# Optimization experiments

Hardware: AMD Instinct MI355X
Metric: run time of the kernel (lower is better)

Reference implementation:

```python
import jax, jax.numpy as jnp
import numpy as np

N, C, H, DIN = 200_000, 16, 64, 40  # nodes in level, max children, hidden_dim, input_dim+type_count
NEG = -1e9

def setup_inputs() -> dict:
    key = jax.random.key(0)
    ks = jax.random.split(key, 10)
    s = lambda k, shp, f=0.1: jax.random.normal(k, shp, jnp.float32) * f
    return {
        'node_features': jax.random.normal(ks[0], (N, 1, DIN), jnp.float32),
        'child_hiddens': jax.random.normal(ks[1], (N, C, H), jnp.float32),
        'A_c': jax.random.uniform(ks[2], (N, C, C), jnp.float32),  # edge present where > 0.5
        'child_count': jax.random.randint(ks[3], (N,), 1, C + 1, jnp.int32),
        'W': s(ks[4], (H, H)),
        'a_src': s(ks[5], (H,)),
        'a_dst': s(ks[6], (H,)),
        'Wx': s(ks[7], (DIN, 3 * H)),
        'Wh_g': s(ks[8], (H, 3 * H)),
        'b': jnp.zeros((3 * H,), jnp.float32),
    }

def reference(node_features, child_hiddens, A_c, child_count, W, a_src, a_dst, Wx, Wh_g, b):
    # --- GraphAttentionLayer over padded child adjacency ---
    Wh = jnp.einsum('nch,hk->nck', child_hiddens, W)            # [N,C,H]
    src = Wh @ a_src                                             # [N,C]
    dst = Wh @ a_dst                                             # [N,C]
    e = jax.nn.leaky_relu(src[:, :, None] + dst[:, None, :], 0.2)  # [N,C,C]
    valid = jnp.arange(C)[None, :] < child_count[:, None]        # [N,C] real (non-padded) children
    mask = (A_c > 0.5) & valid[:, None, :] & valid[:, :, None]
    attn = jax.nn.softmax(jnp.where(mask, e, NEG), axis=-1)
    h_msg = jax.nn.elu(jnp.einsum('nij,njh->nih', attn, Wh))     # [N,C,H]
    # --- MaxpoolReadoutLayer masked by child count ---
    pooled = jnp.max(jnp.where(valid[:, :, None], h_msg, NEG), axis=1, keepdims=True)  # [N,1,H]
    # --- GatedRecurrentUnit update ---
    gx = node_features @ Wx + b                                  # [N,1,3H]
    gh = pooled @ Wh_g                                           # [N,1,3H]
    xz, xr, xn = jnp.split(gx, 3, axis=-1)
    hz, hr, hn = jnp.split(gh, 3, axis=-1)
    z = jax.nn.sigmoid(xz + hz)
    r = jax.nn.sigmoid(xr + hr)
    n = jnp.tanh(xn + r * hn)
    hiddens = (1.0 - z) * n + z * pooled                         # [N,1,H]
    return hiddens
```

## Files before the change

### kernel.cpp

```cpp
#include <hip/hip_runtime.h>

typedef __attribute__((ext_vector_type(8))) short bf16x8;
typedef __attribute__((ext_vector_type(4))) float f32x4;

__device__ __forceinline__ unsigned short f2bf(float f) {
  unsigned u = __builtin_bit_cast(unsigned, f);
  u += 0x7fffu + ((u >> 16) & 1u);
  return (unsigned short)(u >> 16);
}
__device__ __forceinline__ float bf2f(unsigned short s) {
  unsigned u = ((unsigned)s) << 16;
  return __builtin_bit_cast(float, u);
}
__device__ __forceinline__ bf16x8 zero8() {
  bf16x8 r;
#pragma unroll
  for (int i = 0; i < 8; ++i) r[i] = 0;
  return r;
}

__global__ __launch_bounds__(256, 2) void rann_fused(
    const float* __restrict__ nf, const float* __restrict__ ch,
    const float* __restrict__ Ac, const int* __restrict__ ccnt,
    const float* __restrict__ W, const float* __restrict__ a_src,
    const float* __restrict__ a_dst, const float* __restrict__ Wx,
    const float* __restrict__ Whg, const float* __restrict__ bias,
    float* __restrict__ out, int N) {
  __shared__ __align__(16) unsigned short whgT[192][72];
  __shared__ __align__(16) unsigned short wxT[192][72];
  __shared__ __align__(16) float b_lds[192];
  __shared__ __align__(16) float srcdst[4][32];
  __shared__ __align__(16) unsigned short wh_t[4][64][16];
  __shared__ __align__(16) unsigned short pooledb[4][16][72];

  const int tid = threadIdx.x;
  for (int idx = tid; idx < 192 * 64; idx += 256) {
    const int col = idx % 192, k = idx / 192;
    whgT[col][k] = f2bf(Whg[k * 192 + col]);
    wxT[col][k] = (k < 40) ? f2bf(Wx[k * 192 + col]) : (unsigned short)0;
  }
  if (tid < 192) b_lds[tid] = bias[tid];
  __syncthreads();

  const int lane = tid & 63;
  const int w = tid >> 6;
  const int q = lane >> 4;
  const int m16 = lane & 15;

  bf16x8 wfrag[2][4];
#pragma unroll
  for (int t = 0; t < 2; ++t)
#pragma unroll
    for (int u = 0; u < 4; ++u) {
      bf16x8 f;
#pragma unroll
      for (int j = 0; j < 8; ++j)
        f[j] = (short)f2bf(W[(32 * t + 8 * q + j) * 64 + 16 * u + m16]);
      wfrag[t][u] = f;
    }
  float asv[4], adv[4];
#pragma unroll
  for (int u = 0; u < 4; ++u) {
    asv[u] = a_src[16 * u + m16];
    adv[u] = a_dst[16 * u + m16];
  }

  const int gwave = blockIdx.x * 4 + w;
  const int stride = gridDim.x * 4;
  const int nbatch = N >> 4;
  for (int bidx = gwave; bidx < nbatch; bidx += stride) {
    const int nb = bidx << 4;
    for (int s = 0; s < 16; ++s) {
      const int n = nb + s;
      const int cc = ccnt[n];
      bf16x8 afA[2];
#pragma unroll
      for (int t = 0; t < 2; ++t) {
        const float* p = ch + (size_t)n * 1024 + m16 * 64 + 32 * t + 8 * q;
        f32x4 v0 = *(const f32x4*)p;
        f32x4 v1 = *(const f32x4*)(p + 4);
        bf16x8 f;
#pragma unroll
        for (int j = 0; j < 4; ++j) {
          f[j] = (short)f2bf(v0[j]);
          f[j + 4] = (short)f2bf(v1[j]);
        }
        afA[t] = f;
      }
      f32x4 acc[4];
#pragma unroll
      for (int u = 0; u < 4; ++u) acc[u] = (f32x4){0.f, 0.f, 0.f, 0.f};
#pragma unroll
      for (int t = 0; t < 2; ++t)
#pragma unroll
        for (int u = 0; u < 4; ++u)
          acc[u] = __builtin_amdgcn_mfma_f32_16x16x32_bf16(afA[t], wfrag[t][u], acc[u], 0, 0, 0);

      float ps[4], pd[4];
#pragma unroll
      for (int r = 0; r < 4; ++r) {
        ps[r] = acc[0][r] * asv[0] + acc[1][r] * asv[1] + acc[2][r] * asv[2] + acc[3][r] * asv[3];
        pd[r] = acc[0][r] * adv[0] + acc[1][r] * adv[1] + acc[2][r] * adv[2] + acc[3][r] * adv[3];
      }
#pragma unroll
      for (int m = 1; m < 16; m <<= 1) {
#pragma unroll
        for (int r = 0; r < 4; ++r) {
          ps[r] += __shfl_xor(ps[r], m);
          pd[r] += __shfl_xor(pd[r], m);
        }
      }
      if (m16 == 0) {
        *(f32x4*)&srcdst[w][4 * q] = (f32x4){ps[0], ps[1], ps[2], ps[3]};
        *(f32x4*)&srcdst[w][16 + 4 * q] = (f32x4){pd[0], pd[1], pd[2], pd[3]};
      }
#pragma unroll
      for (int u = 0; u < 4; ++u) {
        uint2 v;
        v.x = (unsigned)f2bf(acc[u][0]) | ((unsigned)f2bf(acc[u][1]) << 16);
        v.y = (unsigned)f2bf(acc[u][2]) | ((unsigned)f2bf(acc[u][3]) << 16);
        *(uint2*)&wh_t[w][16 * u + m16][4 * q] = v;
      }
      __threadfence_block();

      const int qe = q & 1;
      const float srcv = srcdst[w][m16];
      f32x4 d0 = *(const f32x4*)&srcdst[w][16 + 8 * qe];
      f32x4 d1 = *(const f32x4*)&srcdst[w][16 + 8 * qe + 4];
      const float* ap = Ac + (size_t)n * 256 + m16 * 16 + 8 * qe;
      f32x4 a0 = *(const f32x4*)ap;
      f32x4 a1 = *(const f32x4*)(ap + 4);
      float p8[8];
      float rmax = -3.0e38f;
#pragma unroll
      for (int jj = 0; jj < 8; ++jj) {
        const float dstv = (jj < 4) ? d0[jj] : d1[jj - 4];
        const float av = (jj < 4) ? a0[jj] : a1[jj - 4];
        const float x = srcv + dstv;
        const float e = fmaxf(x, 0.2f * x);
        const bool msk = (av > 0.5f) && (m16 < cc) && ((8 * qe + jj) < cc);
        p8[jj] = msk ? e : -1.0e9f;
        rmax = fmaxf(rmax, p8[jj]);
      }
      rmax = fmaxf(rmax, __shfl_xor(rmax, 16));
      float psum = 0.f;
#pragma unroll
      for (int jj = 0; jj < 8; ++jj) {
        p8[jj] = __expf(p8[jj] - rmax);
        psum += p8[jj];
      }
      psum += __shfl_xor(psum, 16);
      const float inv = 1.0f / psum;
      bf16x8 afrag2 = zero8();
      if (q < 2) {
#pragma unroll
        for (int jj = 0; jj < 8; ++jj) afrag2[jj] = (short)f2bf(p8[jj] * inv);
      }
      f32x4 acc2[4];
#pragma unroll
      for (int u = 0; u < 4; ++u) {
        bf16x8 bf2 = zero8();
        if (q < 2) bf2 = *(const bf16x8*)&wh_t[w][16 * u + m16][8 * q];
        f32x4 z4 = (f32x4){0.f, 0.f, 0.f, 0.f};
        acc2[u] = __builtin_amdgcn_mfma_f32_16x16x32_bf16(afrag2, bf2, z4, 0, 0, 0);
      }
#pragma unroll
      for (int u = 0; u < 4; ++u) {
        float pm = -1.0e9f;
#pragma unroll
        for (int r = 0; r < 4; ++r) {
          const float v = acc2[u][r];
          const float ev = v > 0.f ? v : __expf(v) - 1.0f;
          pm = fmaxf(pm, (4 * q + r) < cc ? ev : -1.0e9f);
        }
        pm = fmaxf(pm, __shfl_xor(pm, 16));
        pm = fmaxf(pm, __shfl_xor(pm, 32));
        if (q == 0) pooledb[w][s][16 * u + m16] = f2bf(pm);
      }
    }
    __threadfence_block();

    bf16x8 afP[2];
#pragma unroll
    for (int t = 0; t < 2; ++t)
      afP[t] = *(const bf16x8*)&pooledb[w][m16][32 * t + 8 * q];
    bf16x8 afX[2];
    {
      const float* p = nf + (size_t)(nb + m16) * 40 + 8 * q;
      f32x4 v0 = *(const f32x4*)p;
      f32x4 v1 = *(const f32x4*)(p + 4);
      bf16x8 f;
#pragma unroll
      for (int j = 0; j < 4; ++j) {
        f[j] = (short)f2bf(v0[j]);
        f[j + 4] = (short)f2bf(v1[j]);
      }
      afX[0] = f;
      afX[1] = zero8();
      if (q == 0) {
        const float* p1 = nf + (size_t)(nb + m16) * 40 + 32;
        f32x4 w0 = *(const f32x4*)p1;
        f32x4 w1 = *(const f32x4*)(p1 + 4);
        bf16x8 g;
#pragma unroll
        for (int j = 0; j < 4; ++j) {
          g[j] = (short)f2bf(w0[j]);
          g[j + 4] = (short)f2bf(w1[j]);
        }
        afX[1] = g;
      }
    }
    f32x4 accS[8], accX4[4], accH4[4];
#pragma unroll
    for (int u = 0; u < 8; ++u) accS[u] = (f32x4){0.f, 0.f, 0.f, 0.f};
#pragma unroll
    for (int u = 0; u < 4; ++u) {
      accX4[u] = (f32x4){0.f, 0.f, 0.f, 0.f};
      accH4[u] = (f32x4){0.f, 0.f, 0.f, 0.f};
    }
#pragma unroll
    for (int u = 0; u < 8; ++u) {
      const int row = 16 * u + m16;
#pragma unroll
      for (int t = 0; t < 2; ++t) {
        accS[u] = __builtin_amdgcn_mfma_f32_16x16x32_bf16(
            afP[t], *(const bf16x8*)&whgT[row][32 * t + 8 * q], accS[u], 0, 0, 0);
        accS[u] = __builtin_amdgcn_mfma_f32_16x16x32_bf16(
            afX[t], *(const bf16x8*)&wxT[row][32 * t + 8 * q], accS[u], 0, 0, 0);
      }
    }
#pragma unroll
    for (int u = 0; u < 4; ++u) {
      const int row = 128 + 16 * u + m16;
#pragma unroll
      for (int t = 0; t < 2; ++t) {
        accH4[u] = __builtin_amdgcn_mfma_f32_16x16x32_bf16(
            afP[t], *(const bf16x8*)&whgT[row][32 * t + 8 * q], accH4[u], 0, 0, 0);
        accX4[u] = __builtin_amdgcn_mfma_f32_16x16x32_bf16(
            afX[t], *(const bf16x8*)&wxT[row][32 * t + 8 * q], accX4[u], 0, 0, 0);
      }
    }
#pragma unroll
    for (int u = 0; u < 4; ++u) {
      const int col = 16 * u + m16;
      const float bz = b_lds[col];
      const float br = b_lds[64 + col];
      const float bn = b_lds[128 + col];
#pragma unroll
      for (int r = 0; r < 4; ++r) {
        const int nl = 4 * q + r;
        const float z = 1.0f / (1.0f + __expf(-(accS[u][r] + bz)));
        const float rg = 1.0f / (1.0f + __expf(-(accS[u + 4][r] + br)));
        const float nn = tanhf(accX4[u][r] + bn + rg * accH4[u][r]);
        const float pv = bf2f(pooledb[w][nl][col]);
        out[(size_t)(nb + nl) * 64 + col] = (1.0f - z) * nn + z * pv;
      }
    }
  }
}

extern "C" void kernel_launch(void* const* d_in, const int* in_sizes, int n_in,
                              void* d_out, int out_size, void* d_ws, size_t ws_size,
                              hipStream_t stream) {
  const float* nf = (const float*)d_in[0];
  const float* ch = (const float*)d_in[1];
  const float* Ac = (const float*)d_in[2];
  const int* ccnt = (const int*)d_in[3];
  const float* W = (const float*)d_in[4];
  const float* a_src = (const float*)d_in[5];
  const float* a_dst = (const float*)d_in[6];
  const float* Wx = (const float*)d_in[7];
  const float* Whg = (const float*)d_in[8];
  const float* bias = (const float*)d_in[9];
  float* out = (float*)d_out;
  const int N = in_sizes[3];
  const int nbatch = N >> 4;
  int blocks = 625;
  if (blocks > (nbatch + 3) / 4) blocks = (nbatch + 3) / 4;
  if (blocks < 1) blocks = 1;
  hipLaunchKernelGGL(rann_fused, dim3(blocks), dim3(256), 0, stream,
                     nf, ch, Ac, ccnt, W, a_src, a_dst, Wx, Whg, bias, out, N);
}
```

Measured before the change: 1.500 ms.

## Split fused kernel into GAT-pool and GRU kernels with prefetch and folded attention vectors

```diff
diff --git a/kernel.cpp b/kernel.cpp
--- a/kernel.cpp
+++ b/kernel.cpp
@@ -8,9 +8,18 @@
   u += 0x7fffu + ((u >> 16) & 1u);
   return (unsigned short)(u >> 16);
 }
-__device__ __forceinline__ float bf2f(unsigned short s) {
-  unsigned u = ((unsigned)s) << 16;
-  return __builtin_bit_cast(float, u);
+__device__ __forceinline__ unsigned cvtpk(float lo, float hi) {
+  unsigned r;
+  asm("v_cvt_pk_bf16_f32 %0, %1, %2" : "=v"(r) : "v"(lo), "v"(hi));
+  return r;
+}
+__device__ __forceinline__ bf16x8 pk8(f32x4 a, f32x4 b) {
+  union { unsigned u[4]; bf16x8 v; } r;
+  r.u[0] = cvtpk(a[0], a[1]);
+  r.u[1] = cvtpk(a[2], a[3]);
+  r.u[2] = cvtpk(b[0], b[1]);
+  r.u[3] = cvtpk(b[2], b[3]);
+  return r.v;
 }
 __device__ __forceinline__ bf16x8 zero8() {
   bf16x8 r;
@@ -19,124 +28,106 @@
   return r;
 }
 
-__global__ __launch_bounds__(256, 2) void rann_fused(
-    const float* __restrict__ nf, const float* __restrict__ ch,
-    const float* __restrict__ Ac, const int* __restrict__ ccnt,
-    const float* __restrict__ W, const float* __restrict__ a_src,
-    const float* __restrict__ a_dst, const float* __restrict__ Wx,
-    const float* __restrict__ Whg, const float* __restrict__ bias,
-    float* __restrict__ out, int N) {
-  __shared__ __align__(16) unsigned short whgT[192][72];
-  __shared__ __align__(16) unsigned short wxT[192][72];
-  __shared__ __align__(16) float b_lds[192];
-  __shared__ __align__(16) float srcdst[4][32];
+__global__ __launch_bounds__(256, 3) void gat_pool(
+    const float* __restrict__ ch, const float* __restrict__ Ac,
+    const int* __restrict__ ccnt, const float* __restrict__ W,
+    const float* __restrict__ a_src, const float* __restrict__ a_dst,
+    float* __restrict__ pooled, int N) {
+  __shared__ __align__(16) unsigned short wT[64][72];
+  __shared__ __align__(16) float wa[128];
+  __shared__ __align__(16) float dstl[4][16];
   __shared__ __align__(16) unsigned short wh_t[4][64][16];
-  __shared__ __align__(16) unsigned short pooledb[4][16][72];
 
   const int tid = threadIdx.x;
-  for (int idx = tid; idx < 192 * 64; idx += 256) {
-    const int col = idx % 192, k = idx / 192;
-    whgT[col][k] = f2bf(Whg[k * 192 + col]);
-    wxT[col][k] = (k < 40) ? f2bf(Wx[k * 192 + col]) : (unsigned short)0;
-  }
-  if (tid < 192) b_lds[tid] = bias[tid];
+  for (int idx = tid; idx < 64 * 64; idx += 256) {
+    wT[idx & 63][idx >> 6] = f2bf(W[idx]);
+  }
+  if (tid < 128) {
+    const int k = tid & 63;
+    const float* av = (tid < 64) ? a_src : a_dst;
+    float s = 0.f;
+    for (int h = 0; h < 64; ++h) s += W[k * 64 + h] * av[h];
+    wa[tid] = s;
+  }
   __syncthreads();
 
   const int lane = tid & 63;
   const int w = tid >> 6;
   const int q = lane >> 4;
   const int m16 = lane & 15;
-
-  bf16x8 wfrag[2][4];
-#pragma unroll
-  for (int t = 0; t < 2; ++t)
-#pragma unroll
-    for (int u = 0; u < 4; ++u) {
-      bf16x8 f;
-#pragma unroll
-      for (int j = 0; j < 8; ++j)
-        f[j] = (short)f2bf(W[(32 * t + 8 * q + j) * 64 + 16 * u + m16]);
-      wfrag[t][u] = f;
-    }
-  float asv[4], adv[4];
-#pragma unroll
-  for (int u = 0; u < 4; ++u) {
-    asv[u] = a_src[16 * u + m16];
-    adv[u] = a_dst[16 * u + m16];
-  }
+  const int qe = q & 1;
+
+  const f32x4 ws0a = *(const f32x4*)&wa[8 * q];
+  const f32x4 ws0b = *(const f32x4*)&wa[8 * q + 4];
+  const f32x4 ws1a = *(const f32x4*)&wa[32 + 8 * q];
+  const f32x4 ws1b = *(const f32x4*)&wa[36 + 8 * q];
+  const f32x4 wd0a = *(const f32x4*)&wa[64 + 8 * q];
+  const f32x4 wd0b = *(const f32x4*)&wa[68 + 8 * q];
+  const f32x4 wd1a = *(const f32x4*)&wa[96 + 8 * q];
+  const f32x4 wd1b = *(const f32x4*)&wa[100 + 8 * q];
 
   const int gwave = blockIdx.x * 4 + w;
   const int stride = gridDim.x * 4;
   const int nbatch = N >> 4;
   for (int bidx = gwave; bidx < nbatch; bidx += stride) {
     const int nb = bidx << 4;
+    const float* pch = ch + (size_t)nb * 1024 + m16 * 64 + 8 * q;
+    const float* pac = Ac + (size_t)nb * 256 + m16 * 16 + 8 * qe;
+    const int ccv = ccnt[nb + m16];
+    f32x4 c0 = *(const f32x4*)pch;
+    f32x4 c1 = *(const f32x4*)(pch + 4);
+    f32x4 c2 = *(const f32x4*)(pch + 32);
+    f32x4 c3 = *(const f32x4*)(pch + 36);
+    f32x4 A0 = *(const f32x4*)pac;
+    f32x4 A1 = *(const f32x4*)(pac + 4);
+
     for (int s = 0; s < 16; ++s) {
       const int n = nb + s;
-      const int cc = ccnt[n];
-      bf16x8 afA[2];
-#pragma unroll
-      for (int t = 0; t < 2; ++t) {
-        const float* p = ch + (size_t)n * 1024 + m16 * 64 + 32 * t + 8 * q;
-        f32x4 v0 = *(const f32x4*)p;
-        f32x4 v1 = *(const f32x4*)(p + 4);
-        bf16x8 f;
-#pragma unroll
-        for (int j = 0; j < 4; ++j) {
-          f[j] = (short)f2bf(v0[j]);
-          f[j + 4] = (short)f2bf(v1[j]);
-        }
-        afA[t] = f;
-      }
+      const int cc = __builtin_amdgcn_readlane(ccv, s);
+      f32x4 nc0, nc1, nc2, nc3, nA0, nA1;
+      if (s < 15) {
+        const float* p2 = pch + (size_t)(s + 1) * 1024;
+        nc0 = *(const f32x4*)p2;
+        nc1 = *(const f32x4*)(p2 + 4);
+        nc2 = *(const f32x4*)(p2 + 32);
+        nc3 = *(const f32x4*)(p2 + 36);
+        const float* a2 = pac + (size_t)(s + 1) * 256;
+        nA0 = *(const f32x4*)a2;
+        nA1 = *(const f32x4*)(a2 + 4);
+      }
+      float ps = 0.f, pd = 0.f;
+#pragma unroll
+      for (int j = 0; j < 4; ++j) {
+        ps += c0[j] * ws0a[j] + c1[j] * ws0b[j] + c2[j] * ws1a[j] + c3[j] * ws1b[j];
+        pd += c0[j] * wd0a[j] + c1[j] * wd0b[j] + c2[j] * wd1a[j] + c3[j] * wd1b[j];
+      }
+      ps += __shfl_xor(ps, 16);
+      ps += __shfl_xor(ps, 32);
+      pd += __shfl_xor(pd, 16);
+      pd += __shfl_xor(pd, 32);
+      if (q == 0) dstl[w][m16] = pd;
+      const bf16x8 afA0 = pk8(c0, c1);
+      const bf16x8 afA1 = pk8(c2, c3);
       f32x4 acc[4];
 #pragma unroll
       for (int u = 0; u < 4; ++u) acc[u] = (f32x4){0.f, 0.f, 0.f, 0.f};
 #pragma unroll
-      for (int t = 0; t < 2; ++t)
-#pragma unroll
-        for (int u = 0; u < 4; ++u)
-          acc[u] = __builtin_amdgcn_mfma_f32_16x16x32_bf16(afA[t], wfrag[t][u], acc[u], 0, 0, 0);
-
-      float ps[4], pd[4];
-#pragma unroll
-      for (int r = 0; r < 4; ++r) {
-        ps[r] = acc[0][r] * asv[0] + acc[1][r] * asv[1] + acc[2][r] * asv[2] + acc[3][r] * asv[3];
-        pd[r] = acc[0][r] * adv[0] + acc[1][r] * adv[1] + acc[2][r] * adv[2] + acc[3][r] * adv[3];
-      }
-#pragma unroll
-      for (int m = 1; m < 16; m <<= 1) {
-#pragma unroll
-        for (int r = 0; r < 4; ++r) {
-          ps[r] += __shfl_xor(ps[r], m);
-          pd[r] += __shfl_xor(pd[r], m);
-        }
-      }
-      if (m16 == 0) {
-        *(f32x4*)&srcdst[w][4 * q] = (f32x4){ps[0], ps[1], ps[2], ps[3]};
-        *(f32x4*)&srcdst[w][16 + 4 * q] = (f32x4){pd[0], pd[1], pd[2], pd[3]};
-      }
-#pragma unroll
       for (int u = 0; u < 4; ++u) {
-        uint2 v;
-        v.x = (unsigned)f2bf(acc[u][0]) | ((unsigned)f2bf(acc[u][1]) << 16);
-        v.y = (unsigned)f2bf(acc[u][2]) | ((unsigned)f2bf(acc[u][3]) << 16);
-        *(uint2*)&wh_t[w][16 * u + m16][4 * q] = v;
+        acc[u] = __builtin_amdgcn_mfma_f32_16x16x32_bf16(
+            afA0, *(const bf16x8*)&wT[16 * u + m16][8 * q], acc[u], 0, 0, 0);
+        acc[u] = __builtin_amdgcn_mfma_f32_16x16x32_bf16(
+            afA1, *(const bf16x8*)&wT[16 * u + m16][32 + 8 * q], acc[u], 0, 0, 0);
       }
       __threadfence_block();
-
-      const int qe = q & 1;
-      const float srcv = srcdst[w][m16];
-      f32x4 d0 = *(const f32x4*)&srcdst[w][16 + 8 * qe];
-      f32x4 d1 = *(const f32x4*)&srcdst[w][16 + 8 * qe + 4];
-      const float* ap = Ac + (size_t)n * 256 + m16 * 16 + 8 * qe;
-      f32x4 a0 = *(const f32x4*)ap;
-      f32x4 a1 = *(const f32x4*)(ap + 4);
+      const f32x4 d0 = *(const f32x4*)&dstl[w][8 * qe];
+      const f32x4 d1 = *(const f32x4*)&dstl[w][8 * qe + 4];
       float p8[8];
       float rmax = -3.0e38f;
 #pragma unroll
       for (int jj = 0; jj < 8; ++jj) {
         const float dstv = (jj < 4) ? d0[jj] : d1[jj - 4];
-        const float av = (jj < 4) ? a0[jj] : a1[jj - 4];
-        const float x = srcv + dstv;
+        const float av = (jj < 4) ? A0[jj] : A1[jj - 4];
+        const float x = ps + dstv;
         const float e = fmaxf(x, 0.2f * x);
         const bool msk = (av > 0.5f) && (m16 < cc) && ((8 * qe + jj) < cc);
         p8[jj] = msk ? e : -1.0e9f;
@@ -153,63 +144,107 @@
       const float inv = 1.0f / psum;
       bf16x8 afrag2 = zero8();
       if (q < 2) {
-#pragma unroll
-        for (int jj = 0; jj < 8; ++jj) afrag2[jj] = (short)f2bf(p8[jj] * inv);
-      }
-      f32x4 acc2[4];
+        union { unsigned u[4]; bf16x8 v; } r;
+#pragma unroll
+        for (int jj = 0; jj < 4; ++jj)
+          r.u[jj] = cvtpk(p8[2 * jj] * inv, p8[2 * jj + 1] * inv);
+        afrag2 = r.v;
+      }
+#pragma unroll
+      for (int u = 0; u < 4; ++u) {
+        uint2 v;
+        v.x = cvtpk(acc[u][0], acc[u][1]);
+        v.y = cvtpk(acc[u][2], acc[u][3]);
+        *(uint2*)&wh_t[w][16 * u + m16][4 * q] = v;
+      }
+      __threadfence_block();
+      float pmv[4];
 #pragma unroll
       for (int u = 0; u < 4; ++u) {
         bf16x8 bf2 = zero8();
         if (q < 2) bf2 = *(const bf16x8*)&wh_t[w][16 * u + m16][8 * q];
-        f32x4 z4 = (f32x4){0.f, 0.f, 0.f, 0.f};
-        acc2[u] = __builtin_amdgcn_mfma_f32_16x16x32_bf16(afrag2, bf2, z4, 0, 0, 0);
-      }
-#pragma unroll
-      for (int u = 0; u < 4; ++u) {
+        const f32x4 z4 = (f32x4){0.f, 0.f, 0.f, 0.f};
+        const f32x4 h4 =
+            __builtin_amdgcn_mfma_f32_16x16x32_bf16(afrag2, bf2, z4, 0, 0, 0);
         float pm = -1.0e9f;
 #pragma unroll
         for (int r = 0; r < 4; ++r) {
-          const float v = acc2[u][r];
+          const float v = h4[r];
           const float ev = v > 0.f ? v : __expf(v) - 1.0f;
           pm = fmaxf(pm, (4 * q + r) < cc ? ev : -1.0e9f);
         }
         pm = fmaxf(pm, __shfl_xor(pm, 16));
         pm = fmaxf(pm, __shfl_xor(pm, 32));
-        if (q == 0) pooledb[w][s][16 * u + m16] = f2bf(pm);
-      }
-    }
-    __threadfence_block();
-
+        pmv[u] = pm;
+      }
+      const float sel = (q == 0) ? pmv[0] : (q == 1) ? pmv[1] : (q == 2) ? pmv[2] : pmv[3];
+      pooled[(size_t)n * 64 + lane] = sel;
+      if (s < 15) {
+        c0 = nc0; c1 = nc1; c2 = nc2; c3 = nc3;
+        A0 = nA0; A1 = nA1;
+      }
+    }
+  }
+}
+
+__global__ __launch_bounds__(256, 3) void gru_update(
+    const float* __restrict__ nf, const float* __restrict__ Wx,
+    const float* __restrict__ Whg, const float* __restrict__ bias,
+    float* hid, int N) {
+  __shared__ __align__(16) unsigned short whgT[192][72];
+  __shared__ __align__(16) unsigned short wxT[192][40];
+  __shared__ __align__(16) float b_lds[192];
+
+  const int tid = threadIdx.x;
+  for (int idx = tid; idx < 192 * 64; idx += 256) {
+    const int col = idx % 192, k = idx / 192;
+    whgT[col][k] = f2bf(Whg[k * 192 + col]);
+    if (k < 40) wxT[col][k] = f2bf(Wx[k * 192 + col]);
+  }
+  if (tid < 192) b_lds[tid] = bias[tid];
+  __syncthreads();
+
+  const int lane = tid & 63;
+  const int w = tid >> 6;
+  const int q = lane >> 4;
+  const int m16 = lane & 15;
+
+  const int gwave = blockIdx.x * 4 + w;
+  const int stride = gridDim.x * 4;
+  const int nbatch = N >> 4;
+  for (int bidx = gwave; bidx < nbatch; bidx += stride) {
+    const int nb = bidx << 4;
     bf16x8 afP[2];
-#pragma unroll
-    for (int t = 0; t < 2; ++t)
-      afP[t] = *(const bf16x8*)&pooledb[w][m16][32 * t + 8 * q];
+    {
+      const float* p = hid + (size_t)(nb + m16) * 64 + 8 * q;
+      const f32x4 v0 = *(const f32x4*)p;
+      const f32x4 v1 = *(const f32x4*)(p + 4);
+      const f32x4 v2 = *(const f32x4*)(p + 32);
+      const f32x4 v3 = *(const f32x4*)(p + 36);
+      afP[0] = pk8(v0, v1);
+      afP[1] = pk8(v2, v3);
+    }
     bf16x8 afX[2];
     {
       const float* p = nf + (size_t)(nb + m16) * 40 + 8 * q;
-      f32x4 v0 = *(const f32x4*)p;
-      f32x4 v1 = *(const f32x4*)(p + 4);
-      bf16x8 f;
-#pragma unroll
-      for (int j = 0; j < 4; ++j) {
-        f[j] = (short)f2bf(v0[j]);
-        f[j + 4] = (short)f2bf(v1[j]);
-      }
-      afX[0] = f;
+      const f32x4 v0 = *(const f32x4*)p;
+      const f32x4 v1 = *(const f32x4*)(p + 4);
+      afX[0] = pk8(v0, v1);
       afX[1] = zero8();
       if (q == 0) {
         const float* p1 = nf + (size_t)(nb + m16) * 40 + 32;
-        f32x4 w0 = *(const f32x4*)p1;
-        f32x4 w1 = *(const f32x4*)(p1 + 4);
-        bf16x8 g;
-#pragma unroll
-        for (int j = 0; j < 4; ++j) {
-          g[j] = (short)f2bf(w0[j]);
-          g[j + 4] = (short)f2bf(w1[j]);
-        }
-        afX[1] = g;
-      }
-    }
+        const f32x4 w0 = *(const f32x4*)p1;
+        const f32x4 w1 = *(const f32x4*)(p1 + 4);
+        afX[1] = pk8(w0, w1);
+      }
+    }
+    float pv[4][4];
+#pragma unroll
+    for (int u = 0; u < 4; ++u)
+#pragma unroll
+      for (int r = 0; r < 4; ++r)
+        pv[u][r] = hid[(size_t)(nb + 4 * q + r) * 64 + 16 * u + m16];
+
     f32x4 accS[8], accX4[4], accH4[4];
 #pragma unroll
     for (int u = 0; u < 8; ++u) accS[u] = (f32x4){0.f, 0.f, 0.f, 0.f};
@@ -221,24 +256,26 @@
 #pragma unroll
     for (int u = 0; u < 8; ++u) {
       const int row = 16 * u + m16;
-#pragma unroll
-      for (int t = 0; t < 2; ++t) {
-        accS[u] = __builtin_amdgcn_mfma_f32_16x16x32_bf16(
-            afP[t], *(const bf16x8*)&whgT[row][32 * t + 8 * q], accS[u], 0, 0, 0);
-        accS[u] = __builtin_amdgcn_mfma_f32_16x16x32_bf16(
-            afX[t], *(const bf16x8*)&wxT[row][32 * t + 8 * q], accS[u], 0, 0, 0);
-      }
+      accS[u] = __builtin_amdgcn_mfma_f32_16x16x32_bf16(
+          afP[0], *(const bf16x8*)&whgT[row][8 * q], accS[u], 0, 0, 0);
+      accS[u] = __builtin_amdgcn_mfma_f32_16x16x32_bf16(
+          afX[0], *(const bf16x8*)&wxT[row][8 * q], accS[u], 0, 0, 0);
+      accS[u] = __builtin_amdgcn_mfma_f32_16x16x32_bf16(
+          afP[1], *(const bf16x8*)&whgT[row][32 + 8 * q], accS[u], 0, 0, 0);
+      const bf16x8 bx1 = (q == 0) ? *(const bf16x8*)&wxT[row][32] : zero8();
+      accS[u] = __builtin_amdgcn_mfma_f32_16x16x32_bf16(afX[1], bx1, accS[u], 0, 0, 0);
     }
 #pragma unroll
     for (int u = 0; u < 4; ++u) {
       const int row = 128 + 16 * u + m16;
-#pragma unroll
-      for (int t = 0; t < 2; ++t) {
-        accH4[u] = __builtin_amdgcn_mfma_f32_16x16x32_bf16(
-            afP[t], *(const bf16x8*)&whgT[row][32 * t + 8 * q], accH4[u], 0, 0, 0);
-        accX4[u] = __builtin_amdgcn_mfma_f32_16x16x32_bf16(
-            afX[t], *(const bf16x8*)&wxT[row][32 * t + 8 * q], accX4[u], 0, 0, 0);
-      }
+      accH4[u] = __builtin_amdgcn_mfma_f32_16x16x32_bf16(
+          afP[0], *(const bf16x8*)&whgT[row][8 * q], accH4[u], 0, 0, 0);
+      accX4[u] = __builtin_amdgcn_mfma_f32_16x16x32_bf16(
+          afX[0], *(const bf16x8*)&wxT[row][8 * q], accX4[u], 0, 0, 0);
+      accH4[u] = __builtin_amdgcn_mfma_f32_16x16x32_bf16(
+          afP[1], *(const bf16x8*)&whgT[row][32 + 8 * q], accH4[u], 0, 0, 0);
+      const bf16x8 bx1 = (q == 0) ? *(const bf16x8*)&wxT[row][32] : zero8();
+      accX4[u] = __builtin_amdgcn_mfma_f32_16x16x32_bf16(afX[1], bx1, accX4[u], 0, 0, 0);
     }
 #pragma unroll
     for (int u = 0; u < 4; ++u) {
@@ -248,12 +285,10 @@
       const float bn = b_lds[128 + col];
 #pragma unroll
       for (int r = 0; r < 4; ++r) {
-        const int nl = 4 * q + r;
         const float z = 1.0f / (1.0f + __expf(-(accS[u][r] + bz)));
         const float rg = 1.0f / (1.0f + __expf(-(accS[u + 4][r] + br)));
         const float nn = tanhf(accX4[u][r] + bn + rg * accH4[u][r]);
-        const float pv = bf2f(pooledb[w][nl][col]);
-        out[(size_t)(nb + nl) * 64 + col] = (1.0f - z) * nn + z * pv;
+        hid[(size_t)(nb + 4 * q + r) * 64 + col] = (1.0f - z) * nn + z * pv[u][r];
       }
     }
   }
@@ -275,9 +310,16 @@
   float* out = (float*)d_out;
   const int N = in_sizes[3];
   const int nbatch = N >> 4;
-  int blocks = 625;
-  if (blocks > (nbatch + 3) / 4) blocks = (nbatch + 3) / 4;
-  if (blocks < 1) blocks = 1;
-  hipLaunchKernelGGL(rann_fused, dim3(blocks), dim3(256), 0, stream,
-                     nf, ch, Ac, ccnt, W, a_src, a_dst, Wx, Whg, bias, out, N);
-}
+
+  int blocksA = 1563;
+  if (blocksA > (nbatch + 3) / 4) blocksA = (nbatch + 3) / 4;
+  if (blocksA < 1) blocksA = 1;
+  hipLaunchKernelGGL(gat_pool, dim3(blocksA), dim3(256), 0, stream,
+                     ch, Ac, ccnt, W, a_src, a_dst, out, N);
+
+  int blocksB = 782;
+  if (blocksB > (nbatch + 3) / 4) blocksB = (nbatch + 3) / 4;
+  if (blocksB < 1) blocksB = 1;
+  hipLaunchKernelGGL(gru_update, dim3(blocksB), dim3(256), 0, stream,
+                     nf, Wx, Whg, bias, out, N);
+}
```

New measurement: 1.354 ms. -9.7%, faster.
